# Optimization experiments

Hardware: AMD Instinct MI355X
Metric: run time of the kernel (lower is better)

## Reference

```python
import jax, jax.numpy as jnp
import numpy as np

N = 50000   # nodes
E = 800000  # edges (before self loops)
NEG_SLOPE = 0.2
EPS_BN = 1e-5
EPS_SM = 1e-16  # PyG softmax denominator epsilon


def gat_conv(x, src, dst, W, att_src, att_dst, bias, heads, ch):
    n = x.shape[0]
    xh = (x @ W).reshape(n, heads, ch)                       # [N,H,C]
    a_src = jnp.sum(xh * att_src, axis=-1)                   # [N,H]
    a_dst = jnp.sum(xh * att_dst, axis=-1)                   # [N,H]
    e = a_src[src] + a_dst[dst]                              # [E,H]
    e = jax.nn.leaky_relu(e, NEG_SLOPE)
    m = jax.ops.segment_max(e, dst, num_segments=n)          # segment softmax
    ex = jnp.exp(e - m[dst])
    denom = jax.ops.segment_sum(ex, dst, num_segments=n)
    alpha = ex / (denom[dst] + EPS_SM)                       # [E,H]
    msg = alpha[:, :, None] * xh[src]                        # [E,H,C]
    out = jax.ops.segment_sum(msg, dst, num_segments=n)      # [N,H,C]
    return out.reshape(n, heads * ch) + bias


def batch_norm(x, gamma, beta):
    mu = jnp.mean(x, axis=0)
    var = jnp.mean((x - mu) ** 2, axis=0)
    return (x - mu) * jax.lax.rsqrt(var + EPS_BN) * gamma + beta


def setup_inputs() -> dict:
    key = jax.random.key(0)
    ks = jax.random.split(key, 16)
    d = {}
    d['x'] = jax.random.normal(ks[0], (N, 128), jnp.float32)
    d['edge_index'] = jax.random.randint(ks[1], (2, E), 0, N, dtype=jnp.int64)
    d['W1'] = jax.random.normal(ks[2], (128, 256), jnp.float32) * 0.1
    d['as1'] = jax.random.normal(ks[3], (2, 128), jnp.float32) * 0.1
    d['ad1'] = jax.random.normal(ks[4], (2, 128), jnp.float32) * 0.1
    d['b1'] = jax.random.normal(ks[5], (256,), jnp.float32) * 0.1
    d['g1'] = jnp.ones((256,), jnp.float32)
    d['be1'] = jnp.zeros((256,), jnp.float32)
    d['W2'] = jax.random.normal(ks[6], (256, 128), jnp.float32) * 0.1
    d['as2'] = jax.random.normal(ks[7], (2, 64), jnp.float32) * 0.1
    d['ad2'] = jax.random.normal(ks[8], (2, 64), jnp.float32) * 0.1
    d['b2'] = jax.random.normal(ks[9], (128,), jnp.float32) * 0.1
    d['g2'] = jnp.ones((128,), jnp.float32)
    d['be2'] = jnp.zeros((128,), jnp.float32)
    d['W3'] = jax.random.normal(ks[10], (128, 128), jnp.float32) * 0.1
    d['as3'] = jax.random.normal(ks[11], (2, 64), jnp.float32) * 0.1
    d['ad3'] = jax.random.normal(ks[12], (2, 64), jnp.float32) * 0.1
    d['b3'] = jax.random.normal(ks[13], (128,), jnp.float32) * 0.1
    d['lw'] = jax.random.normal(ks[14], (128, 64), jnp.float32) * 0.1
    d['lb'] = jnp.zeros((64,), jnp.float32)
    return d


def reference(x, edge_index, W1, as1, ad1, b1, g1, be1,
              W2, as2, ad2, b2, g2, be2,
              W3, as3, ad3, b3, lw, lb):
    # add self loops (PyG GATConv default add_self_loops=True)
    loops = jnp.arange(N, dtype=edge_index.dtype)
    src = jnp.concatenate([edge_index[0], loops])
    dst = jnp.concatenate([edge_index[1], loops])

    h = jax.nn.relu(gat_conv(x, src, dst, W1, as1, ad1, b1, 2, 128))   # [N,256]
    h = batch_norm(h, g1, be1)
    h = jax.nn.relu(gat_conv(h, src, dst, W2, as2, ad2, b2, 2, 64))    # [N,128]
    h = batch_norm(h, g2, be2)
    h = jax.nn.relu(gat_conv(h, src, dst, W3, as3, ad3, b3, 2, 64))    # [N,128]
    return h @ lw + lb                                                 # [N,64]
```

## Files before the change

### kernel.cpp

```cpp
#include <hip/hip_runtime.h>
#include <hip/hip_bf16.h>

#define NEG_SLOPE 0.2f
#define EPS_BN 1e-5f
#define EPS_SM 1e-16f
#define CAP 128

typedef __bf16 bf16x8 __attribute__((ext_vector_type(8)));
typedef __bf16 bf16x4 __attribute__((ext_vector_type(4)));
typedef float floatx4 __attribute__((ext_vector_type(4)));

__device__ __forceinline__ float leaky(float x) { return x > 0.f ? x : NEG_SLOPE * x; }

__global__ void k_init(const int* __restrict__ ei, int* __restrict__ flag,
                       int* __restrict__ zbase, int zwords, int e) {
    if (blockIdx.x == 0) {
        __shared__ int cnt_s[256];
        int i = threadIdx.x;
        int nz = (2 * i + 1 < 2 * e && ei[2 * i + 1] != 0) ? 1 : 0;
        cnt_s[i] = nz;
        __syncthreads();
        for (int off = 128; off > 0; off >>= 1) {
            if (i < off) cnt_s[i] += cnt_s[i + off];
            __syncthreads();
        }
        if (i == 0) *flag = (cnt_s[0] < 128) ? 1 : 0;
        return;
    }
    int g = (blockIdx.x - 1) * 256 + threadIdx.x;
    int stride = (gridDim.x - 1) * 256;
    for (int k = g; k < zwords; k += stride) zbase[k] = 0;
}

__global__ void k_hist_wconv(const int* __restrict__ ei, const int* __restrict__ flag,
                             int* __restrict__ deg, int* __restrict__ col, int e, int ebase,
                             const float* __restrict__ W1, __bf16* __restrict__ Wb1,
                             const float* __restrict__ W2, __bf16* __restrict__ Wb2,
                             const float* __restrict__ W3, __bf16* __restrict__ Wb3) {
    int g = threadIdx.x + blockIdx.x * blockDim.x;
    if (g < e) {
        bool is64 = (*flag) != 0;
        int s = is64 ? ei[2 * g] : ei[g];
        int d = is64 ? ei[2 * (e + g)] : ei[e + g];
        int r = atomicAdd(&deg[d], 1);
        if (r < CAP) col[((size_t)d << 7) + r] = s;
    } else {
        int idx = g - ebase;
        if (idx >= 0 && idx < 32768) {
            int mm = idx >> 7, kk = idx & 127;
            Wb1[idx] = (__bf16)W1[(size_t)kk * 256 + mm];
        } else if (idx < 65536) {
            int i2 = idx - 32768;
            int mm = i2 >> 8, kk = i2 & 255;
            Wb2[i2] = (__bf16)W2[(size_t)kk * 128 + mm];
        } else if (idx < 81920) {
            int i3 = idx - 65536;
            int mm = i3 >> 7, kk = i3 & 127;
            Wb3[i3] = (__bf16)W3[(size_t)kk * 128 + mm];
        }
    }
}

template <int K, int LC, bool BF16IN, int NT>
__global__ __launch_bounds__(256) void k_gemm(const void* __restrict__ Ain,
                                              const __bf16* __restrict__ Bt,
                                              __bf16* __restrict__ Cb, int n, int M,
                                              const float* __restrict__ bnsums,
                                              const float* __restrict__ gam,
                                              const float* __restrict__ bet,
                                              const float* __restrict__ att_s,
                                              const float* __restrict__ att_d,
                                              float* __restrict__ asrc,
                                              float* __restrict__ adst) {
    __shared__ __align__(16) __bf16 As[128][72];
    __shared__ __align__(16) __bf16 Bs[NT * 16][72];
    __shared__ float sc_lds[K], sh_lds[K];
    const int row0 = blockIdx.y * 128, col0 = blockIdx.x * (NT * 16);
    const int lane = threadIdx.x & 63, w = threadIdx.x >> 6;
    const int m = lane & 15, quad = lane >> 4;

    if (bnsums) {
        for (int c = threadIdx.x; c < K; c += 256) {
            float mean = bnsums[c] / n;
            float var = bnsums[256 + c] / n - mean * mean;
            float sc = gam[c] * rsqrtf(var + EPS_BN);
            sc_lds[c] = sc;
            sh_lds[c] = bet[c] - mean * sc;
        }
        __syncthreads();
    }

    floatx4 acc[2][NT];
#pragma unroll
    for (int i = 0; i < 2; ++i)
#pragma unroll
        for (int j = 0; j < NT; ++j) acc[i][j] = (floatx4)0.f;

    const int sr = threadIdx.x >> 1;
    const int sk = (threadIdx.x & 1) * 32;

    for (int kc = 0; kc < K; kc += 64) {
        {
            int grow = row0 + sr;
            if (grow < n) {
                if (BF16IN) {
                    const __bf16* p = (const __bf16*)Ain + (size_t)grow * K + kc + sk;
#pragma unroll
                    for (int q = 0; q < 4; ++q) {
                        bf16x8 vv = *reinterpret_cast<const bf16x8*>(p + q * 8);
                        if (bnsums) {
                            int c = kc + sk + q * 8;
                            bf16x8 r;
#pragma unroll
                            for (int e2 = 0; e2 < 8; ++e2)
                                r[e2] = (__bf16)((float)vv[e2] * sc_lds[c + e2] + sh_lds[c + e2]);
                            vv = r;
                        }
                        *reinterpret_cast<bf16x8*>(&As[sr][sk + q * 8]) = vv;
                    }
                } else {
                    const float* p = (const float*)Ain + (size_t)grow * K + kc + sk;
#pragma unroll
                    for (int q = 0; q < 8; ++q) {
                        float4 v = *reinterpret_cast<const float4*>(p + q * 4);
                        bf16x4 cv = {(__bf16)v.x, (__bf16)v.y, (__bf16)v.z, (__bf16)v.w};
                        *reinterpret_cast<bf16x4*>(&As[sr][sk + q * 4]) = cv;
                    }
                }
            } else {
#pragma unroll
                for (int q = 0; q < 4; ++q)
                    *reinterpret_cast<bf16x8*>(&As[sr][sk + q * 8]) = (bf16x8)(__bf16)0.f;
            }
        }
        if (NT == 8) {
            const __bf16* p = Bt + (size_t)(col0 + sr) * K + kc + sk;
#pragma unroll
            for (int q = 0; q < 4; ++q)
                *reinterpret_cast<bf16x8*>(&Bs[sr][sk + q * 8]) =
                    *reinterpret_cast<const bf16x8*>(p + q * 8);
        } else {
            int sr4 = threadIdx.x >> 2, sk4 = (threadIdx.x & 3) * 16;
            const __bf16* p = Bt + (size_t)(col0 + sr4) * K + kc + sk4;
            *reinterpret_cast<bf16x8*>(&Bs[sr4][sk4]) = *reinterpret_cast<const bf16x8*>(p);
            *reinterpret_cast<bf16x8*>(&Bs[sr4][sk4 + 8]) = *reinterpret_cast<const bf16x8*>(p + 8);
        }
        __syncthreads();
#pragma unroll
        for (int ks = 0; ks < 64; ks += 32) {
            bf16x8 a0 = *reinterpret_cast<const bf16x8*>(&As[w * 32 + m][ks + quad * 8]);
            bf16x8 a1 = *reinterpret_cast<const bf16x8*>(&As[w * 32 + 16 + m][ks + quad * 8]);
#pragma unroll
            for (int nt = 0; nt < NT; ++nt) {
                bf16x8 b = *reinterpret_cast<const bf16x8*>(&Bs[nt * 16 + m][ks + quad * 8]);
                acc[0][nt] = __builtin_amdgcn_mfma_f32_16x16x32_bf16(a0, b, acc[0][nt], 0, 0, 0);
                acc[1][nt] = __builtin_amdgcn_mfma_f32_16x16x32_bf16(a1, b, acc[1][nt], 0, 0, 0);
            }
        }
        __syncthreads();
    }
#pragma unroll
    for (int mt = 0; mt < 2; ++mt)
#pragma unroll
        for (int nt = 0; nt < NT; ++nt)
#pragma unroll
            for (int r = 0; r < 4; ++r) {
                int row = row0 + w * 32 + mt * 16 + quad * 4 + r;
                if (row < n) Cb[(size_t)row * M + col0 + nt * 16 + m] = (__bf16)acc[mt][nt][r];
            }
    {
        float asv[NT], adv[NT];
#pragma unroll
        for (int nt = 0; nt < NT; ++nt) {
            int c = col0 + nt * 16 + m;
            asv[nt] = att_s[c];
            adv[nt] = att_d[c];
        }
        const int h = (col0 >> LC) & 1;
#pragma unroll
        for (int mt = 0; mt < 2; ++mt)
#pragma unroll
            for (int r = 0; r < 4; ++r) {
                int row = row0 + w * 32 + mt * 16 + quad * 4 + r;
                float pa = 0.f, pb = 0.f;
#pragma unroll
                for (int nt = 0; nt < NT; ++nt) {
                    float v = acc[mt][nt][r];
                    pa += v * asv[nt];
                    pb += v * adv[nt];
                }
#pragma unroll
                for (int off = 1; off <= 8; off <<= 1) {
                    pa += __shfl_xor(pa, off);
                    pb += __shfl_xor(pb, off);
                }
                if (m == 0 && row < n) {
                    asrc[2 * row + h] = pa;
                    adst[2 * row + h] = pb;
                }
            }
    }
}

__global__ __launch_bounds__(256) void k_lin(const float* __restrict__ A,
                                             const float* __restrict__ lw,
                                             const float* __restrict__ lb,
                                             float* __restrict__ out, int n) {
    __shared__ __align__(16) __bf16 Ahi[64][136];
    __shared__ __align__(16) __bf16 Alo[64][136];
    __shared__ __align__(16) __bf16 Bhi[64][136];
    const int row0 = blockIdx.x * 64;
    const int lane = threadIdx.x & 63, w = threadIdx.x >> 6;
    const int m = lane & 15, quad = lane >> 4;
    floatx4 acc[4];
#pragma unroll
    for (int i = 0; i < 4; ++i) acc[i] = (floatx4)0.f;
    {
        int sr = threadIdx.x >> 2, sk0 = (threadIdx.x & 3) * 32;
        int grow = row0 + sr;
#pragma unroll
        for (int q = 0; q < 8; ++q) {
            float4 v = make_float4(0.f, 0.f, 0.f, 0.f);
            if (grow < n) v = *reinterpret_cast<const float4*>(A + (size_t)grow * 128 + sk0 + q * 4);
            float vv[4] = {v.x, v.y, v.z, v.w};
#pragma unroll
            for (int i = 0; i < 4; ++i) {
                __bf16 h = (__bf16)vv[i];
                Ahi[sr][sk0 + q * 4 + i] = h;
                Alo[sr][sk0 + q * 4 + i] = (__bf16)(vv[i] - (float)h);
            }
        }
    }
    {
        int k0 = threadIdx.x >> 1, m0 = (threadIdx.x & 1) * 32;
#pragma unroll
        for (int q = 0; q < 8; ++q) {
            float4 v = *reinterpret_cast<const float4*>(lw + (size_t)k0 * 64 + m0 + q * 4);
            float vv[4] = {v.x, v.y, v.z, v.w};
#pragma unroll
            for (int i = 0; i < 4; ++i) Bhi[m0 + q * 4 + i][k0] = (__bf16)vv[i];
        }
    }
    __syncthreads();
#pragma unroll
    for (int ks = 0; ks < 128; ks += 32) {
        bf16x8 ah = *reinterpret_cast<const bf16x8*>(&Ahi[w * 16 + m][ks + quad * 8]);
        bf16x8 al = *reinterpret_cast<const bf16x8*>(&Alo[w * 16 + m][ks + quad * 8]);
#pragma unroll
        for (int nt = 0; nt < 4; ++nt) {
            bf16x8 bh = *reinterpret_cast<const bf16x8*>(&Bhi[nt * 16 + m][ks + quad * 8]);
            acc[nt] = __builtin_amdgcn_mfma_f32_16x16x32_bf16(ah, bh, acc[nt], 0, 0, 0);
            acc[nt] = __builtin_amdgcn_mfma_f32_16x16x32_bf16(al, bh, acc[nt], 0, 0, 0);
        }
    }
#pragma unroll
    for (int nt = 0; nt < 4; ++nt)
#pragma unroll
        for (int r = 0; r < 4; ++r) {
            int row = row0 + w * 16 + quad * 4 + r;
            int c = nt * 16 + m;
            if (row < n) out[(size_t)row * 64 + c] = acc[nt][r] + lb[c];
        }
}

template <int C, bool OUTBF16>
__global__ __launch_bounds__(256) void k_agg(const __bf16* __restrict__ xh,
                                             const float* __restrict__ asrc,
                                             const float* __restrict__ adst,
                                             const int* __restrict__ degv,
                                             const int* __restrict__ col,
                                             const float* __restrict__ bias,
                                             void* __restrict__ outv, int n) {
    constexpr int F = 2 * C;
    constexpr int G = F / 8;
    constexpr int NG = 64 / G;
    constexpr int GSH = (G == 32) ? 5 : 4;
    __shared__ float4 slots[4][80];
    const int widx = threadIdx.x >> 6;
    const int node = blockIdx.x * 4 + widx;
    const int lane = threadIdx.x & 63;
    if (node >= n) return;
    const int t = lane & (G - 1);
    const int g = lane >> GSH;
    const bool h1 = (t * 8) >= C;
    if (lane >= 48) slots[widx][lane + 16] = make_float4(0.f, 0.f, 0.f, 0.f);
    const int* crow = col + ((size_t)node << 7);
    const int deg = min(degv[node], CAP);
    const float2 adv = *reinterpret_cast<const float2*>(adst + 2 * node);
    const float2 asv = *reinterpret_cast<const float2*>(asrc + 2 * node);
    const float es0 = leaky(asv.x + adv.x), es1 = leaky(asv.y + adv.y);
    float acc[8] = {};
    float d0 = 0.f, d1 = 0.f;
    for (int base = 0; base < deg; base += 64) {
        const int cnt = min(64, deg - base);
        float4 sv = make_float4(0.f, 0.f, 0.f, 0.f);
        if (lane < cnt) {
            int s = crow[base + lane];
            float2 av = *reinterpret_cast<const float2*>(asrc + 2 * s);
            float w0 = __expf(leaky(av.x + adv.x));
            float w1 = __expf(leaky(av.y + adv.y));
            d0 += w0; d1 += w1;
            sv = make_float4(__int_as_float(s * (F * 2)), w0, w1, 0.f);
        }
        slots[widx][lane] = sv;
        for (int j = g; j < cnt; j += 4 * NG) {
            float4 s0 = slots[widx][j];
            float4 s1 = slots[widx][j + NG];
            float4 s2 = slots[widx][j + 2 * NG];
            float4 s3 = slots[widx][j + 3 * NG];
            const char* xb = (const char*)xh;
            bf16x8 v0 = *reinterpret_cast<const bf16x8*>(xb + (unsigned)__float_as_int(s0.x) + t * 16);
            bf16x8 v1 = *reinterpret_cast<const bf16x8*>(xb + (unsigned)__float_as_int(s1.x) + t * 16);
            bf16x8 v2 = *reinterpret_cast<const bf16x8*>(xb + (unsigned)__float_as_int(s2.x) + t * 16);
            bf16x8 v3 = *reinterpret_cast<const bf16x8*>(xb + (unsigned)__float_as_int(s3.x) + t * 16);
            float w0 = h1 ? s0.z : s0.y;
            float w1 = h1 ? s1.z : s1.y;
            float w2 = h1 ? s2.z : s2.y;
            float w3 = h1 ? s3.z : s3.y;
#pragma unroll
            for (int q = 0; q < 8; ++q)
                acc[q] += w0 * (float)v0[q] + w1 * (float)v1[q] +
                          w2 * (float)v2[q] + w3 * (float)v3[q];
        }
    }
#pragma unroll
    for (int off = 1; off <= 32; off <<= 1) {
        d0 += __shfl_xor(d0, off);
        d1 += __shfl_xor(d1, off);
    }
#pragma unroll
    for (int q = 0; q < 8; ++q) {
#pragma unroll
        for (int off = G; off < 64; off <<= 1) acc[q] += __shfl_xor(acc[q], off);
    }
    float exs0 = __expf(es0), exs1 = __expf(es1);
    d0 += exs0; d1 += exs1;
    {
        float ws = h1 ? exs1 : exs0;
        bf16x8 v = *reinterpret_cast<const bf16x8*>(xh + (size_t)node * F + t * 8);
#pragma unroll
        for (int q = 0; q < 8; ++q) acc[q] += ws * (float)v[q];
    }
    float inv = 1.0f / ((h1 ? d1 : d0) + EPS_SM);
    float o[8];
#pragma unroll
    for (int q = 0; q < 8; ++q) o[q] = fmaxf(acc[q] * inv + bias[t * 8 + q], 0.f);
    if (g == 0) {
        if constexpr (OUTBF16) {
            __bf16* po = (__bf16*)outv + (size_t)node * F + t * 8;
            bf16x8 st;
#pragma unroll
            for (int q = 0; q < 8; ++q) st[q] = (__bf16)o[q];
            *reinterpret_cast<bf16x8*>(po) = st;
        } else {
            float* po = (float*)outv + (size_t)node * F + t * 8;
            *reinterpret_cast<float4*>(po) = make_float4(o[0], o[1], o[2], o[3]);
            *reinterpret_cast<float4*>(po + 4) = make_float4(o[4], o[5], o[6], o[7]);
        }
    }
}

template <typename T>
__global__ void k_bn_stats(const T* __restrict__ x, float* __restrict__ sums,
                           float* __restrict__ sqs, int n, int f) {
    int c = threadIdx.x;
    float s = 0.f, q = 0.f;
    for (int r = blockIdx.x; r < n; r += gridDim.x) {
        float v = (float)x[(size_t)r * f + c];
        s += v; q += v * v;
    }
    atomicAdd(&sums[c], s);
    atomicAdd(&sqs[c], q);
}

extern "C" void kernel_launch(void* const* d_in, const int* in_sizes, int n_in,
                              void* d_out, int out_size, void* d_ws, size_t ws_size,
                              hipStream_t stream) {
    const float* x   = (const float*)d_in[0];
    const int*   ei  = (const int*)d_in[1];
    const float* W1  = (const float*)d_in[2];
    const float* as1 = (const float*)d_in[3];
    const float* ad1 = (const float*)d_in[4];
    const float* b1  = (const float*)d_in[5];
    const float* g1  = (const float*)d_in[6];
    const float* be1 = (const float*)d_in[7];
    const float* W2  = (const float*)d_in[8];
    const float* as2 = (const float*)d_in[9];
    const float* ad2 = (const float*)d_in[10];
    const float* b2  = (const float*)d_in[11];
    const float* g2  = (const float*)d_in[12];
    const float* be2 = (const float*)d_in[13];
    const float* W3  = (const float*)d_in[14];
    const float* as3 = (const float*)d_in[15];
    const float* ad3 = (const float*)d_in[16];
    const float* b3  = (const float*)d_in[17];
    const float* lw  = (const float*)d_in[18];
    const float* lb  = (const float*)d_in[19];
    float* outp = (float*)d_out;

    const int n = in_sizes[0] / 128;
    const int e = in_sizes[1] / 2;

    char* w = (char*)d_ws;
    size_t off = 0;
    auto alloc = [&](size_t bytes) -> void* {
        void* p = w + off;
        off += (bytes + 255) & ~(size_t)255;
        return p;
    };
    __bf16* xhb = (__bf16*)alloc((size_t)n * 256 * 2);
    __bf16* h1b = (__bf16*)alloc((size_t)n * 256 * 2);
    __bf16* h2b = (__bf16*)alloc((size_t)n * 128 * 2);
    float*  h3f = (float*)alloc((size_t)n * 128 * 4);
    int* colb   = (int*)alloc((size_t)n * CAP * 4);
    __bf16* Wb1 = (__bf16*)alloc(256 * 128 * 2);
    __bf16* Wb2 = (__bf16*)alloc(128 * 256 * 2);
    __bf16* Wb3 = (__bf16*)alloc(128 * 128 * 2);
    int* flag   = (int*)alloc(256);
    float* as1p = (float*)alloc((size_t)n * 2 * 4);
    float* ad1p = (float*)alloc((size_t)n * 2 * 4);
    float* as2p = (float*)alloc((size_t)n * 2 * 4);
    float* ad2p = (float*)alloc((size_t)n * 2 * 4);
    float* as3p = (float*)alloc((size_t)n * 2 * 4);
    float* ad3p = (float*)alloc((size_t)n * 2 * 4);
    char* zb_begin = (char*)(w + off);
    int* deg    = (int*)alloc((size_t)n * 4);
    float* bn1  = (float*)alloc(512 * 4);
    float* bn2  = (float*)alloc(512 * 4);
    char* zb_end = (char*)(w + off);
    const int zwords = (int)((zb_end - zb_begin) / 4);

    k_init<<<65, 256, 0, stream>>>(ei, flag, (int*)zb_begin, zwords, e);

    const int ebase = ((e + 255) / 256) * 256;
    const int histblocks = ebase / 256 + 320;
    k_hist_wconv<<<histblocks, 256, 0, stream>>>(ei, flag, deg, colb, e, ebase,
                                                 W1, Wb1, W2, Wb2, W3, Wb3);

    const int nwb = (n + 3) / 4;
    const int nrow = (n + 127) / 128;

    k_gemm<128, 7, false, 8><<<dim3(2, nrow), 256, 0, stream>>>(
        x, Wb1, xhb, n, 256, nullptr, nullptr, nullptr, as1, ad1, as1p, ad1p);
    k_agg<128, true><<<nwb, 256, 0, stream>>>(xhb, as1p, ad1p, deg, colb, b1, h1b, n);
    k_bn_stats<__bf16><<<256, 256, 0, stream>>>(h1b, bn1, bn1 + 256, n, 256);

    k_gemm<256, 6, true, 4><<<dim3(2, nrow), 256, 0, stream>>>(
        h1b, Wb2, xhb, n, 128, bn1, g1, be1, as2, ad2, as2p, ad2p);
    k_agg<64, true><<<nwb, 256, 0, stream>>>(xhb, as2p, ad2p, deg, colb, b2, h2b, n);
    k_bn_stats<__bf16><<<256, 128, 0, stream>>>(h2b, bn2, bn2 + 256, n, 128);

    k_gemm<128, 6, true, 4><<<dim3(2, nrow), 256, 0, stream>>>(
        h2b, Wb3, xhb, n, 128, bn2, g2, be2, as3, ad3, as3p, ad3p);
    k_agg<64, false><<<nwb, 256, 0, stream>>>(xhb, as3p, ad3p, deg, colb, b3, h3f, n);

    k_lin<<<(n + 63) / 64, 256, 0, stream>>>(h3f, lw, lb, outp, n);
}
```

Baseline: 461.6 us.

## Make aggregation kernel persistent with software-prefetch of next node's metadata

The GAT aggregation kernel becomes a grid-stride persistent loop capped at 2048 blocks. Each wave prefetches the next node's degree, column indices, attention scalars, source attention values and self features while it processes the current node, to hide the dependent-load latency chain at the start of every node. The cost is more live registers (with launch bounds asking for 6 blocks per CU), fewer resident waves, and possible load imbalance across the fixed grid.

```diff
diff --git a/kernel.cpp b/kernel.cpp
--- a/kernel.cpp
+++ b/kernel.cpp
@@ -264,99 +264,158 @@
 }
 
 template <int C, bool OUTBF16>
-__global__ __launch_bounds__(256) void k_agg(const __bf16* __restrict__ xh,
-                                             const float* __restrict__ asrc,
-                                             const float* __restrict__ adst,
-                                             const int* __restrict__ degv,
-                                             const int* __restrict__ col,
-                                             const float* __restrict__ bias,
-                                             void* __restrict__ outv, int n) {
+__global__ __launch_bounds__(256, 6) void k_agg(const __bf16* __restrict__ xh,
+                                                const float* __restrict__ asrc,
+                                                const float* __restrict__ adst,
+                                                const int* __restrict__ degv,
+                                                const int* __restrict__ col,
+                                                const float* __restrict__ bias,
+                                                void* __restrict__ outv, int n) {
     constexpr int F = 2 * C;
     constexpr int G = F / 8;
     constexpr int NG = 64 / G;
     constexpr int GSH = (G == 32) ? 5 : 4;
-    __shared__ float4 slots[4][80];
+    __shared__ float4 slots[4][64];
     const int widx = threadIdx.x >> 6;
-    const int node = blockIdx.x * 4 + widx;
     const int lane = threadIdx.x & 63;
-    if (node >= n) return;
     const int t = lane & (G - 1);
     const int g = lane >> GSH;
     const bool h1 = (t * 8) >= C;
-    if (lane >= 48) slots[widx][lane + 16] = make_float4(0.f, 0.f, 0.f, 0.f);
-    const int* crow = col + ((size_t)node << 7);
-    const int deg = min(degv[node], CAP);
-    const float2 adv = *reinterpret_cast<const float2*>(adst + 2 * node);
-    const float2 asv = *reinterpret_cast<const float2*>(asrc + 2 * node);
-    const float es0 = leaky(asv.x + adv.x), es1 = leaky(asv.y + adv.y);
-    float acc[8] = {};
-    float d0 = 0.f, d1 = 0.f;
-    for (int base = 0; base < deg; base += 64) {
-        const int cnt = min(64, deg - base);
-        float4 sv = make_float4(0.f, 0.f, 0.f, 0.f);
-        if (lane < cnt) {
-            int s = crow[base + lane];
-            float2 av = *reinterpret_cast<const float2*>(asrc + 2 * s);
-            float w0 = __expf(leaky(av.x + adv.x));
-            float w1 = __expf(leaky(av.y + adv.y));
-            d0 += w0; d1 += w1;
-            sv = make_float4(__int_as_float(s * (F * 2)), w0, w1, 0.f);
-        }
-        slots[widx][lane] = sv;
-        for (int j = g; j < cnt; j += 4 * NG) {
-            float4 s0 = slots[widx][j];
-            float4 s1 = slots[widx][j + NG];
-            float4 s2 = slots[widx][j + 2 * NG];
-            float4 s3 = slots[widx][j + 3 * NG];
-            const char* xb = (const char*)xh;
-            bf16x8 v0 = *reinterpret_cast<const bf16x8*>(xb + (unsigned)__float_as_int(s0.x) + t * 16);
-            bf16x8 v1 = *reinterpret_cast<const bf16x8*>(xb + (unsigned)__float_as_int(s1.x) + t * 16);
-            bf16x8 v2 = *reinterpret_cast<const bf16x8*>(xb + (unsigned)__float_as_int(s2.x) + t * 16);
-            bf16x8 v3 = *reinterpret_cast<const bf16x8*>(xb + (unsigned)__float_as_int(s3.x) + t * 16);
-            float w0 = h1 ? s0.z : s0.y;
-            float w1 = h1 ? s1.z : s1.y;
-            float w2 = h1 ? s2.z : s2.y;
-            float w3 = h1 ? s3.z : s3.y;
-#pragma unroll
-            for (int q = 0; q < 8; ++q)
-                acc[q] += w0 * (float)v0[q] + w1 * (float)v1[q] +
-                          w2 * (float)v2[q] + w3 * (float)v3[q];
-        }
-    }
-#pragma unroll
-    for (int off = 1; off <= 32; off <<= 1) {
-        d0 += __shfl_xor(d0, off);
-        d1 += __shfl_xor(d1, off);
-    }
-#pragma unroll
-    for (int q = 0; q < 8; ++q) {
-#pragma unroll
-        for (int off = G; off < 64; off <<= 1) acc[q] += __shfl_xor(acc[q], off);
-    }
-    float exs0 = __expf(es0), exs1 = __expf(es1);
-    d0 += exs0; d1 += exs1;
-    {
-        float ws = h1 ? exs1 : exs0;
-        bf16x8 v = *reinterpret_cast<const bf16x8*>(xh + (size_t)node * F + t * 8);
-#pragma unroll
-        for (int q = 0; q < 8; ++q) acc[q] += ws * (float)v[q];
-    }
-    float inv = 1.0f / ((h1 ? d1 : d0) + EPS_SM);
-    float o[8];
-#pragma unroll
-    for (int q = 0; q < 8; ++q) o[q] = fmaxf(acc[q] * inv + bias[t * 8 + q], 0.f);
-    if (g == 0) {
-        if constexpr (OUTBF16) {
-            __bf16* po = (__bf16*)outv + (size_t)node * F + t * 8;
-            bf16x8 st;
-#pragma unroll
-            for (int q = 0; q < 8; ++q) st[q] = (__bf16)o[q];
-            *reinterpret_cast<bf16x8*>(po) = st;
-        } else {
-            float* po = (float*)outv + (size_t)node * F + t * 8;
-            *reinterpret_cast<float4*>(po) = make_float4(o[0], o[1], o[2], o[3]);
-            *reinterpret_cast<float4*>(po + 4) = make_float4(o[4], o[5], o[6], o[7]);
-        }
+    const char* xbt = (const char*)xh + t * 16;
+    const int NW = gridDim.x * 4;
+    int node = blockIdx.x * 4 + widx;
+    if (node >= n) return;
+
+    int deg = min(degv[node], CAP);
+    int scur = col[((size_t)node << 7) + lane];
+    float2 adv = *reinterpret_cast<const float2*>(adst + 2 * node);
+    float2 asv = *reinterpret_cast<const float2*>(asrc + 2 * node);
+    if (lane >= deg) scur = node;
+    float2 avl = *reinterpret_cast<const float2*>(asrc + 2 * scur);
+    bf16x8 vself = *reinterpret_cast<const bf16x8*>(xbt + (size_t)node * (2 * F));
+
+    while (true) {
+        const int nxt = node + NW;
+        const bool hasnxt = nxt < n;
+        int ndeg = 0, nscur = 0;
+        float2 nadv = make_float2(0.f, 0.f), nasv = make_float2(0.f, 0.f);
+        bf16x8 nvself;
+        if (hasnxt) {
+            ndeg = degv[nxt];
+            nscur = col[((size_t)nxt << 7) + lane];
+            nadv = *reinterpret_cast<const float2*>(adst + 2 * nxt);
+            nasv = *reinterpret_cast<const float2*>(asrc + 2 * nxt);
+            nvself = *reinterpret_cast<const bf16x8*>(xbt + (size_t)nxt * (2 * F));
+        }
+
+        const float es0 = leaky(asv.x + adv.x), es1 = leaky(asv.y + adv.y);
+        float acc[8] = {};
+        float d0 = 0.f, d1 = 0.f;
+        {
+            const int cnt = min(deg, 64);
+            float4 sv = make_float4(0.f, 0.f, 0.f, 0.f);
+            if (lane < cnt) {
+                float w0 = __expf(leaky(avl.x + adv.x));
+                float w1 = __expf(leaky(avl.y + adv.y));
+                d0 += w0; d1 += w1;
+                sv = make_float4(__int_as_float(scur * (F * 2)), w0, w1, 0.f);
+            }
+            slots[widx][lane] = sv;
+            for (int j = g; j < cnt; j += 4 * NG) {
+                float4 s0 = slots[widx][j];
+                float4 s1 = slots[widx][j + NG];
+                float4 s2 = slots[widx][j + 2 * NG];
+                float4 s3 = slots[widx][j + 3 * NG];
+                bf16x8 v0 = *reinterpret_cast<const bf16x8*>(xbt + (unsigned)__float_as_int(s0.x));
+                bf16x8 v1 = *reinterpret_cast<const bf16x8*>(xbt + (unsigned)__float_as_int(s1.x));
+                bf16x8 v2 = *reinterpret_cast<const bf16x8*>(xbt + (unsigned)__float_as_int(s2.x));
+                bf16x8 v3 = *reinterpret_cast<const bf16x8*>(xbt + (unsigned)__float_as_int(s3.x));
+                float w0 = h1 ? s0.z : s0.y;
+                float w1 = h1 ? s1.z : s1.y;
+                float w2 = h1 ? s2.z : s2.y;
+                float w3 = h1 ? s3.z : s3.y;
+#pragma unroll
+                for (int q = 0; q < 8; ++q)
+                    acc[q] += w0 * (float)v0[q] + w1 * (float)v1[q] +
+                              w2 * (float)v2[q] + w3 * (float)v3[q];
+            }
+        }
+        if (deg > 64) {
+            const int cnt = deg - 64;
+            int s2i = col[((size_t)node << 7) + 64 + lane];
+            float4 sv = make_float4(0.f, 0.f, 0.f, 0.f);
+            if (lane < cnt) {
+                float2 av = *reinterpret_cast<const float2*>(asrc + 2 * s2i);
+                float w0 = __expf(leaky(av.x + adv.x));
+                float w1 = __expf(leaky(av.y + adv.y));
+                d0 += w0; d1 += w1;
+                sv = make_float4(__int_as_float(s2i * (F * 2)), w0, w1, 0.f);
+            }
+            slots[widx][lane] = sv;
+            for (int j = g; j < cnt; j += 4 * NG) {
+                float4 s0 = slots[widx][j];
+                float4 s1 = slots[widx][j + NG];
+                float4 s2 = slots[widx][j + 2 * NG];
+                float4 s3 = slots[widx][j + 3 * NG];
+                bf16x8 v0 = *reinterpret_cast<const bf16x8*>(xbt + (unsigned)__float_as_int(s0.x));
+                bf16x8 v1 = *reinterpret_cast<const bf16x8*>(xbt + (unsigned)__float_as_int(s1.x));
+                bf16x8 v2 = *reinterpret_cast<const bf16x8*>(xbt + (unsigned)__float_as_int(s2.x));
+                bf16x8 v3 = *reinterpret_cast<const bf16x8*>(xbt + (unsigned)__float_as_int(s3.x));
+                float w0 = h1 ? s0.z : s0.y;
+                float w1 = h1 ? s1.z : s1.y;
+                float w2 = h1 ? s2.z : s2.y;
+                float w3 = h1 ? s3.z : s3.y;
+#pragma unroll
+                for (int q = 0; q < 8; ++q)
+                    acc[q] += w0 * (float)v0[q] + w1 * (float)v1[q] +
+                              w2 * (float)v2[q] + w3 * (float)v3[q];
+            }
+        }
+
+        float2 navl = make_float2(0.f, 0.f);
+        if (hasnxt) {
+            ndeg = min(ndeg, CAP);
+            if (lane >= ndeg) nscur = nxt;
+            navl = *reinterpret_cast<const float2*>(asrc + 2 * nscur);
+        }
+
+#pragma unroll
+        for (int off = 1; off <= 32; off <<= 1) {
+            d0 += __shfl_xor(d0, off);
+            d1 += __shfl_xor(d1, off);
+        }
+#pragma unroll
+        for (int q = 0; q < 8; ++q) {
+#pragma unroll
+            for (int off = G; off < 64; off <<= 1) acc[q] += __shfl_xor(acc[q], off);
+        }
+        float exs0 = __expf(es0), exs1 = __expf(es1);
+        d0 += exs0; d1 += exs1;
+        {
+            float ws = h1 ? exs1 : exs0;
+#pragma unroll
+            for (int q = 0; q < 8; ++q) acc[q] += ws * (float)vself[q];
+        }
+        float inv = 1.0f / ((h1 ? d1 : d0) + EPS_SM);
+        float o[8];
+#pragma unroll
+        for (int q = 0; q < 8; ++q) o[q] = fmaxf(acc[q] * inv + bias[t * 8 + q], 0.f);
+        if (g == 0) {
+            if constexpr (OUTBF16) {
+                __bf16* po = (__bf16*)outv + (size_t)node * F + t * 8;
+                bf16x8 st;
+#pragma unroll
+                for (int q = 0; q < 8; ++q) st[q] = (__bf16)o[q];
+                *reinterpret_cast<bf16x8*>(po) = st;
+            } else {
+                float* po = (float*)outv + (size_t)node * F + t * 8;
+                *reinterpret_cast<float4*>(po) = make_float4(o[0], o[1], o[2], o[3]);
+                *reinterpret_cast<float4*>(po + 4) = make_float4(o[4], o[5], o[6], o[7]);
+            }
+        }
+        if (!hasnxt) return;
+        node = nxt; deg = ndeg; scur = nscur;
+        adv = nadv; asv = nasv; avl = navl; vself = nvself;
     }
 }
 
@@ -437,7 +496,7 @@
     k_hist_wconv<<<histblocks, 256, 0, stream>>>(ei, flag, deg, colb, e, ebase,
                                                  W1, Wb1, W2, Wb2, W3, Wb3);
 
-    const int nwb = (n + 3) / 4;
+    const int nwb = min((n + 3) / 4, 2048);
     const int nrow = (n + 127) / 128;
 
     k_gemm<128, 7, false, 8><<<dim3(2, nrow), 256, 0, stream>>>(
```

New measurement: 510.0 us. 10.5% more time.

## Reorder layer-1 GAT to aggregate raw inputs before the weight GEMM

Applied to the files above, without the earlier changes.

Layer 1 now computes attention logits directly from x using precomputed W1·att vectors, converts x to bf16, and aggregates the 128-wide input features per head (instead of gathering 256-wide projected features). A per-head GEMM with bias and ReLU is then applied to the aggregated result. This roughly halves the bytes gathered per edge in the first aggregation. The cost is an extra pre-pass kernel and a GEMM over a 256-wide aggregated input split by head. Attention logits are also computed from fp32 x rather than from a bf16-rounded projection, which slightly changes the numerics.

```diff
diff --git a/kernel.cpp b/kernel.cpp
--- a/kernel.cpp
+++ b/kernel.cpp
@@ -13,7 +13,9 @@
 __device__ __forceinline__ float leaky(float x) { return x > 0.f ? x : NEG_SLOPE * x; }
 
 __global__ void k_init(const int* __restrict__ ei, int* __restrict__ flag,
-                       int* __restrict__ zbase, int zwords, int e) {
+                       int* __restrict__ zbase, int zwords, int e,
+                       const float* __restrict__ W1, const float* __restrict__ as1,
+                       const float* __restrict__ ad1, float* __restrict__ wsd) {
     if (blockIdx.x == 0) {
         __shared__ int cnt_s[256];
         int i = threadIdx.x;
@@ -27,8 +29,24 @@
         if (i == 0) *flag = (cnt_s[0] < 128) ? 1 : 0;
         return;
     }
+    if (blockIdx.x == 65) {
+        int k = threadIdx.x;
+        if (k < 128) {
+            const float* wr = W1 + (size_t)k * 256;
+            float s0 = 0.f, s1 = 0.f, d0 = 0.f, d1 = 0.f;
+            for (int c = 0; c < 128; ++c) {
+                float w0 = wr[c], w1 = wr[128 + c];
+                s0 += w0 * as1[c];
+                s1 += w1 * as1[128 + c];
+                d0 += w0 * ad1[c];
+                d1 += w1 * ad1[128 + c];
+            }
+            wsd[k] = s0; wsd[128 + k] = s1; wsd[256 + k] = d0; wsd[384 + k] = d1;
+        }
+        return;
+    }
     int g = (blockIdx.x - 1) * 256 + threadIdx.x;
-    int stride = (gridDim.x - 1) * 256;
+    const int stride = 64 * 256;
     for (int k = g; k < zwords; k += stride) zbase[k] = 0;
 }
 
@@ -59,6 +77,205 @@
             Wb3[i3] = (__bf16)W3[(size_t)kk * 128 + mm];
         }
     }
+}
+
+__global__ __launch_bounds__(256) void k_pre(const float* __restrict__ x,
+                                             const float* __restrict__ wsd,
+                                             __bf16* __restrict__ xb,
+                                             float* __restrict__ asp,
+                                             float* __restrict__ adp, int n) {
+    __shared__ float ws[4][128];
+    for (int i = threadIdx.x; i < 512; i += 256) ws[i >> 7][i & 127] = wsd[i];
+    __syncthreads();
+    const int lane = threadIdx.x & 63, widx = threadIdx.x >> 6;
+    const int sub = lane & 7;
+    const int node = blockIdx.x * 32 + widx * 8 + (lane >> 3);
+    if (node >= n) return;
+    const int c0 = sub * 16;
+    const float* xp = x + (size_t)node * 128 + c0;
+    float xv[16];
+#pragma unroll
+    for (int q = 0; q < 4; ++q) {
+        float4 v = *reinterpret_cast<const float4*>(xp + q * 4);
+        xv[q * 4 + 0] = v.x; xv[q * 4 + 1] = v.y; xv[q * 4 + 2] = v.z; xv[q * 4 + 3] = v.w;
+    }
+    float s0 = 0.f, s1 = 0.f, d0 = 0.f, d1 = 0.f;
+#pragma unroll
+    for (int i = 0; i < 16; ++i) {
+        float xi = xv[i];
+        int c = c0 + i;
+        s0 += xi * ws[0][c]; s1 += xi * ws[1][c];
+        d0 += xi * ws[2][c]; d1 += xi * ws[3][c];
+    }
+#pragma unroll
+    for (int off = 1; off <= 4; off <<= 1) {
+        s0 += __shfl_xor(s0, off); s1 += __shfl_xor(s1, off);
+        d0 += __shfl_xor(d0, off); d1 += __shfl_xor(d1, off);
+    }
+    bf16x8 b0, b1;
+#pragma unroll
+    for (int i = 0; i < 8; ++i) { b0[i] = (__bf16)xv[i]; b1[i] = (__bf16)xv[8 + i]; }
+    __bf16* po = xb + (size_t)node * 128 + c0;
+    *reinterpret_cast<bf16x8*>(po) = b0;
+    *reinterpret_cast<bf16x8*>(po + 8) = b1;
+    if (sub == 0) {
+        *reinterpret_cast<float2*>(asp + 2 * node) = make_float2(s0, s1);
+        *reinterpret_cast<float2*>(adp + 2 * node) = make_float2(d0, d1);
+    }
+}
+
+__global__ __launch_bounds__(256) void k_agg_in(const __bf16* __restrict__ xb,
+                                                const float* __restrict__ asrc,
+                                                const float* __restrict__ adst,
+                                                const int* __restrict__ degv,
+                                                const int* __restrict__ col,
+                                                __bf16* __restrict__ aggv, int n) {
+    __shared__ float4 slots[4][80];
+    const int widx = threadIdx.x >> 6;
+    const int node = blockIdx.x * 4 + widx;
+    const int lane = threadIdx.x & 63;
+    if (node >= n) return;
+    const int t = lane & 15;
+    const int g = lane >> 4;
+    if (lane >= 48) slots[widx][lane + 16] = make_float4(0.f, 0.f, 0.f, 0.f);
+    const char* xbt = (const char*)xb + t * 16;
+    const int* crow = col + ((size_t)node << 7);
+    const int deg = min(degv[node], CAP);
+    const float2 adv = *reinterpret_cast<const float2*>(adst + 2 * node);
+    const float2 asv = *reinterpret_cast<const float2*>(asrc + 2 * node);
+    const float es0 = leaky(asv.x + adv.x), es1 = leaky(asv.y + adv.y);
+    float a0[8] = {}, a1[8] = {};
+    float d0 = 0.f, d1 = 0.f;
+    for (int base = 0; base < deg; base += 64) {
+        const int cnt = min(64, deg - base);
+        float4 sv = make_float4(0.f, 0.f, 0.f, 0.f);
+        if (lane < cnt) {
+            int s = crow[base + lane];
+            float2 av = *reinterpret_cast<const float2*>(asrc + 2 * s);
+            float w0 = __expf(leaky(av.x + adv.x));
+            float w1 = __expf(leaky(av.y + adv.y));
+            d0 += w0; d1 += w1;
+            sv = make_float4(__int_as_float(s * 256), w0, w1, 0.f);
+        }
+        slots[widx][lane] = sv;
+        for (int j = g; j < cnt; j += 16) {
+            float4 s0 = slots[widx][j];
+            float4 s1 = slots[widx][j + 4];
+            float4 s2 = slots[widx][j + 8];
+            float4 s3 = slots[widx][j + 12];
+            bf16x8 v0 = *reinterpret_cast<const bf16x8*>(xbt + (unsigned)__float_as_int(s0.x));
+            bf16x8 v1 = *reinterpret_cast<const bf16x8*>(xbt + (unsigned)__float_as_int(s1.x));
+            bf16x8 v2 = *reinterpret_cast<const bf16x8*>(xbt + (unsigned)__float_as_int(s2.x));
+            bf16x8 v3 = *reinterpret_cast<const bf16x8*>(xbt + (unsigned)__float_as_int(s3.x));
+#pragma unroll
+            for (int q = 0; q < 8; ++q) {
+                float f0 = (float)v0[q], f1 = (float)v1[q], f2 = (float)v2[q], f3 = (float)v3[q];
+                a0[q] += s0.y * f0 + s1.y * f1 + s2.y * f2 + s3.y * f3;
+                a1[q] += s0.z * f0 + s1.z * f1 + s2.z * f2 + s3.z * f3;
+            }
+        }
+    }
+#pragma unroll
+    for (int off = 1; off <= 32; off <<= 1) {
+        d0 += __shfl_xor(d0, off);
+        d1 += __shfl_xor(d1, off);
+    }
+#pragma unroll
+    for (int q = 0; q < 8; ++q) {
+#pragma unroll
+        for (int off = 16; off < 64; off <<= 1) {
+            a0[q] += __shfl_xor(a0[q], off);
+            a1[q] += __shfl_xor(a1[q], off);
+        }
+    }
+    float exs0 = __expf(es0), exs1 = __expf(es1);
+    d0 += exs0; d1 += exs1;
+    {
+        bf16x8 v = *reinterpret_cast<const bf16x8*>(xbt + (size_t)node * 256);
+#pragma unroll
+        for (int q = 0; q < 8; ++q) {
+            a0[q] += exs0 * (float)v[q];
+            a1[q] += exs1 * (float)v[q];
+        }
+    }
+    float i0 = 1.0f / (d0 + EPS_SM), i1 = 1.0f / (d1 + EPS_SM);
+    if (g == 0) {
+        bf16x8 st0, st1;
+#pragma unroll
+        for (int q = 0; q < 8; ++q) {
+            st0[q] = (__bf16)(a0[q] * i0);
+            st1[q] = (__bf16)(a1[q] * i1);
+        }
+        __bf16* po = aggv + (size_t)node * 256 + t * 8;
+        *reinterpret_cast<bf16x8*>(po) = st0;
+        *reinterpret_cast<bf16x8*>(po + 128) = st1;
+    }
+}
+
+__global__ __launch_bounds__(256) void k_gemm_ar(const __bf16* __restrict__ A,
+                                                 const __bf16* __restrict__ Bt,
+                                                 const float* __restrict__ bias,
+                                                 __bf16* __restrict__ Cb, int n) {
+    __shared__ __align__(16) __bf16 As[128][72];
+    __shared__ __align__(16) __bf16 Bs[128][72];
+    const int row0 = blockIdx.y * 128, col0 = blockIdx.x * 128;
+    const int h = col0 >> 7;
+    const int lane = threadIdx.x & 63, w = threadIdx.x >> 6;
+    const int m = lane & 15, quad = lane >> 4;
+    floatx4 acc[2][8];
+#pragma unroll
+    for (int i = 0; i < 2; ++i)
+#pragma unroll
+        for (int j = 0; j < 8; ++j) acc[i][j] = (floatx4)0.f;
+    const int sr = threadIdx.x >> 1;
+    const int sk = (threadIdx.x & 1) * 32;
+    for (int kc = 0; kc < 128; kc += 64) {
+        {
+            int grow = row0 + sr;
+            if (grow < n) {
+                const __bf16* p = A + (size_t)grow * 256 + h * 128 + kc + sk;
+#pragma unroll
+                for (int q = 0; q < 4; ++q)
+                    *reinterpret_cast<bf16x8*>(&As[sr][sk + q * 8]) =
+                        *reinterpret_cast<const bf16x8*>(p + q * 8);
+            } else {
+#pragma unroll
+                for (int q = 0; q < 4; ++q)
+                    *reinterpret_cast<bf16x8*>(&As[sr][sk + q * 8]) = (bf16x8)(__bf16)0.f;
+            }
+        }
+        {
+            const __bf16* p = Bt + (size_t)(col0 + sr) * 128 + kc + sk;
+#pragma unroll
+            for (int q = 0; q < 4; ++q)
+                *reinterpret_cast<bf16x8*>(&Bs[sr][sk + q * 8]) =
+                    *reinterpret_cast<const bf16x8*>(p + q * 8);
+        }
+        __syncthreads();
+#pragma unroll
+        for (int ks = 0; ks < 64; ks += 32) {
+            bf16x8 a0 = *reinterpret_cast<const bf16x8*>(&As[w * 32 + m][ks + quad * 8]);
+            bf16x8 a1 = *reinterpret_cast<const bf16x8*>(&As[w * 32 + 16 + m][ks + quad * 8]);
+#pragma unroll
+            for (int nt = 0; nt < 8; ++nt) {
+                bf16x8 b = *reinterpret_cast<const bf16x8*>(&Bs[nt * 16 + m][ks + quad * 8]);
+                acc[0][nt] = __builtin_amdgcn_mfma_f32_16x16x32_bf16(a0, b, acc[0][nt], 0, 0, 0);
+                acc[1][nt] = __builtin_amdgcn_mfma_f32_16x16x32_bf16(a1, b, acc[1][nt], 0, 0, 0);
+            }
+        }
+        __syncthreads();
+    }
+#pragma unroll
+    for (int mt = 0; mt < 2; ++mt)
+#pragma unroll
+        for (int nt = 0; nt < 8; ++nt)
+#pragma unroll
+            for (int r = 0; r < 4; ++r) {
+                int row = row0 + w * 32 + mt * 16 + quad * 4 + r;
+                int c = col0 + nt * 16 + m;
+                if (row < n)
+                    Cb[(size_t)row * 256 + c] = (__bf16)fmaxf(acc[mt][nt][r] + bias[c], 0.f);
+            }
 }
 
 template <int K, int LC, bool BF16IN, int NT>
@@ -413,9 +630,11 @@
     __bf16* h2b = (__bf16*)alloc((size_t)n * 128 * 2);
     float*  h3f = (float*)alloc((size_t)n * 128 * 4);
     int* colb   = (int*)alloc((size_t)n * CAP * 4);
+    __bf16* xb  = (__bf16*)alloc((size_t)n * 128 * 2);
     __bf16* Wb1 = (__bf16*)alloc(256 * 128 * 2);
     __bf16* Wb2 = (__bf16*)alloc(128 * 256 * 2);
     __bf16* Wb3 = (__bf16*)alloc(128 * 128 * 2);
+    float* wsd  = (float*)alloc(512 * 4);
     int* flag   = (int*)alloc(256);
     float* as1p = (float*)alloc((size_t)n * 2 * 4);
     float* ad1p = (float*)alloc((size_t)n * 2 * 4);
@@ -430,7 +649,7 @@
     char* zb_end = (char*)(w + off);
     const int zwords = (int)((zb_end - zb_begin) / 4);
 
-    k_init<<<65, 256, 0, stream>>>(ei, flag, (int*)zb_begin, zwords, e);
+    k_init<<<66, 256, 0, stream>>>(ei, flag, (int*)zb_begin, zwords, e, W1, as1, ad1, wsd);
 
     const int ebase = ((e + 255) / 256) * 256;
     const int histblocks = ebase / 256 + 320;
@@ -440,9 +659,9 @@
     const int nwb = (n + 3) / 4;
     const int nrow = (n + 127) / 128;
 
-    k_gemm<128, 7, false, 8><<<dim3(2, nrow), 256, 0, stream>>>(
-        x, Wb1, xhb, n, 256, nullptr, nullptr, nullptr, as1, ad1, as1p, ad1p);
-    k_agg<128, true><<<nwb, 256, 0, stream>>>(xhb, as1p, ad1p, deg, colb, b1, h1b, n);
+    k_pre<<<(n + 31) / 32, 256, 0, stream>>>(x, wsd, xb, as1p, ad1p, n);
+    k_agg_in<<<nwb, 256, 0, stream>>>(xb, as1p, ad1p, deg, colb, xhb, n);
+    k_gemm_ar<<<dim3(2, nrow), 256, 0, stream>>>(xhb, Wb1, b1, h1b, n);
     k_bn_stats<__bf16><<<256, 256, 0, stream>>>(h1b, bn1, bn1 + 256, n, 256);
 
     k_gemm<256, 6, true, 4><<<dim3(2, nrow), 256, 0, stream>>>(
```

After: 472.6 us. 1.02x slower.
